# Kernel tuning notes

Hardware: AMD Instinct MI355X
Metric: run time of the kernel (lower is better)

The kernel has to match this reference:

```python
import jax, jax.numpy as jnp
import numpy as np

B, T, F = 64, 512, 512
F2, F4 = F // 2, F // 4
NUM_MOVES = 4


def setup_inputs() -> dict:
    key = jax.random.key(0)
    ks = jax.random.split(key, 12)
    s = 0.02
    return {
        "action_type_index": jax.random.randint(ks[0], (B, T), 0, 2, dtype=jnp.int32),
        "autoregressive_embedding": jax.random.normal(ks[1], (B, T, F), jnp.float32),
        "moves": jax.random.normal(ks[2], (B, T, NUM_MOVES, F2), jnp.float32),
        # guarantee each slot has at least one legal move (the torch code would NaN/error otherwise)
        "moves_mask": jax.random.bernoulli(ks[3], 0.7, (B, T, NUM_MOVES)).at[..., 0].set(True),
        "Wq1": s * jax.random.normal(ks[4], (F, F2), jnp.float32),
        "bq1": jnp.zeros((F2,), jnp.float32),
        "Wq2": s * jax.random.normal(ks[5], (F2, F4), jnp.float32),
        "bq2": jnp.zeros((F4,), jnp.float32),
        "Wk1": s * jax.random.normal(ks[6], (F2, F2), jnp.float32),
        "bk1": jnp.zeros((F2,), jnp.float32),
        "Wk2": s * jax.random.normal(ks[7], (F2, F4), jnp.float32),
        "bk2": jnp.zeros((F4,), jnp.float32),
        "Wp": s * jax.random.normal(ks[8], (F2, F), jnp.float32),
        "bp": jnp.zeros((F,), jnp.float32),
    }


def _legal_policy(logits, legal):
    # softmax over last axis that respects the legality mask, same ops as torch version
    l_min = logits.min(axis=-1, keepdims=True)
    l = jnp.where(legal, logits, l_min)
    l = l - l.max(axis=-1, keepdims=True)
    l = l * legal
    e = jnp.where(legal, jnp.exp(l), 0.0)
    return e / e.sum(axis=-1, keepdims=True)


def reference(action_type_index, autoregressive_embedding, moves, moves_mask,
              Wq1, bq1, Wq2, bq2, Wk1, bk1, Wk2, bk2, Wp, bp):
    # mask fixup: if the whole mask is empty, make everything legal (torch scalar-bool indexing)
    mask = jnp.where(moves_mask.sum() == 0, jnp.bool_(True), moves_mask)

    q = jax.nn.relu(autoregressive_embedding @ Wq1 + bq1) @ Wq2 + bq2   # [B,T,F4]
    k = jax.nn.relu(moves @ Wk1 + bk1) @ Wk2 + bk2                       # [B,T,4,F4]
    move_logits = jnp.einsum('btf,btmf->btm', q, k)                      # [B,T,4]

    move_policy = _legal_policy(move_logits, mask)                       # [B,T,4]

    # multinomial sample per (B,T) slot (deterministic key for reproducibility)
    samp_logits = jnp.where(move_policy > 0, jnp.log(move_policy), -1e30)
    idx = jax.random.categorical(jax.random.key(42), samp_logits, axis=-1)  # [B,T] int32
    move_index = idx.reshape(B, T, 1)

    # gather sampled move embedding (each slot gathers from its own 4 moves)
    move_embedding = jnp.take_along_axis(moves, idx[:, :, None, None], axis=2)[:, :, 0, :]  # [B,T,F2]
    projected_move_embedding = move_embedding @ Wp + bp                  # [B,T,F]

    valid = (action_type_index == 0)[..., None]                          # [B,T,1]
    ar_out = jnp.where(valid, autoregressive_embedding + projected_move_embedding,
                       autoregressive_embedding)
    return move_logits, move_policy, move_index, ar_out, projected_move_embedding
```

## Files before the change

kernel.cpp:

```cpp
#include <hip/hip_runtime.h>

#define B_   64
#define T_   512
#define F_   512
#define F2_  256
#define F4_  128
#define R_   32768
#define RM_  131072

typedef __attribute__((ext_vector_type(8))) short bf16x8;
typedef __attribute__((ext_vector_type(4))) float f32x4;

__device__ __forceinline__ void split_bf16(float a, unsigned short& h, unsigned short& l)
{
    unsigned x  = __float_as_uint(a);
    unsigned rh = x + 0x7FFFu + ((x >> 16) & 1u);
    unsigned short hs = (unsigned short)(rh >> 16);
    float fh = __uint_as_float((unsigned)hs << 16);
    float r  = a - fh;
    unsigned y  = __float_as_uint(r);
    unsigned rl = y + 0x7FFFu + ((y >> 16) & 1u);
    h = hs;
    l = (unsigned short)(rl >> 16);
}

template<bool TRANS>
__global__ __launch_bounds__(256)
void repack_kernel(const float* __restrict__ src, int N, int kbits,
                   unsigned short* __restrict__ hi, unsigned short* __restrict__ lo)
{
    int idx = blockIdx.x * 256 + threadIdx.x;
    int K = 1 << kbits;
    int k = idx & (K - 1);
    int n = idx >> kbits;
    float v = TRANS ? src[(size_t)k * N + n] : src[idx];
    unsigned short h, l;
    split_bf16(v, h, l);
    hi[idx] = h; lo[idx] = l;
}

#define LDSPAD 40

template<int KDIM, int NDIM, bool RELU, bool PROJ>
__global__ __launch_bounds__(256, 2)
void gemm_bf16s(const float* __restrict__ A,
                const unsigned short* __restrict__ Wh,
                const unsigned short* __restrict__ Wl,
                const float* __restrict__ bias,
                float* __restrict__ C,
                const float* __restrict__ idxf,
                const float* __restrict__ moves,
                const float* __restrict__ xres,
                const int*   __restrict__ atype,
                float* __restrict__ out_ar)
{
    __shared__ unsigned short AhS[128 * LDSPAD];
    __shared__ unsigned short AlS[128 * LDSPAD];
    __shared__ unsigned short WhS[128 * LDSPAD];
    __shared__ unsigned short WlS[128 * LDSPAD];

    const int tid  = threadIdx.x;
    const int lane = tid & 63;
    const int wid  = tid >> 6;
    const int wr   = wid >> 1;
    const int wc   = wid & 1;
    const int row0 = blockIdx.x * 128;
    const int col0 = blockIdx.y * 128;

    const int sr = tid >> 1;
    const int sc = (tid & 1) * 16;
    const float* arow;
    if constexpr (PROJ) {
        const int slot = row0 + sr;
        const int mi = (int)idxf[slot];
        arow = moves + ((size_t)slot * 4 + mi) * KDIM;
    } else {
        arow = A + (size_t)(row0 + sr) * KDIM;
    }
    const int wn = tid & 127;
    const unsigned short* wrow = ((tid >> 7) ? Wl : Wh) + (size_t)(col0 + wn) * KDIM;
    unsigned short* wdst = (tid >> 7) ? WlS : WhS;

    const int fr   = lane & 15;
    const int fkg  = (lane >> 4) * 8;
    const int aoff = (wr * 64 + fr) * LDSPAD + fkg;
    const int woff = (wc * 64 + fr) * LDSPAD + fkg;

    f32x4 acc[4][4];
#pragma unroll
    for (int i = 0; i < 4; i++)
#pragma unroll
        for (int j = 0; j < 4; j++) acc[i][j] = {0.f, 0.f, 0.f, 0.f};

    float4 pa[4];
    uint4  pw[4];
#pragma unroll
    for (int i = 0; i < 4; i++) pa[i] = *(const float4*)&arow[sc + i * 4];
#pragma unroll
    for (int i = 0; i < 4; i++) pw[i] = *(const uint4*)&wrow[i * 8];

    for (int k0 = 0; k0 < KDIM; k0 += 32) {
        {
            unsigned hw[8], lw[8];
#pragma unroll
            for (int i = 0; i < 4; i++) {
                unsigned short h0, l0, h1, l1;
                split_bf16(pa[i].x, h0, l0);
                split_bf16(pa[i].y, h1, l1);
                hw[i * 2 + 0] = (unsigned)h0 | ((unsigned)h1 << 16);
                lw[i * 2 + 0] = (unsigned)l0 | ((unsigned)l1 << 16);
                split_bf16(pa[i].z, h0, l0);
                split_bf16(pa[i].w, h1, l1);
                hw[i * 2 + 1] = (unsigned)h0 | ((unsigned)h1 << 16);
                lw[i * 2 + 1] = (unsigned)l0 | ((unsigned)l1 << 16);
            }
            *(uint4*)&AhS[sr * LDSPAD + sc]     = (uint4){hw[0], hw[1], hw[2], hw[3]};
            *(uint4*)&AhS[sr * LDSPAD + sc + 8] = (uint4){hw[4], hw[5], hw[6], hw[7]};
            *(uint4*)&AlS[sr * LDSPAD + sc]     = (uint4){lw[0], lw[1], lw[2], lw[3]};
            *(uint4*)&AlS[sr * LDSPAD + sc + 8] = (uint4){lw[4], lw[5], lw[6], lw[7]};
#pragma unroll
            for (int i = 0; i < 4; i++)
                *(uint4*)&wdst[wn * LDSPAD + i * 8] = pw[i];
        }
        __syncthreads();

        if (k0 + 32 < KDIM) {
#pragma unroll
            for (int i = 0; i < 4; i++) pa[i] = *(const float4*)&arow[k0 + 32 + sc + i * 4];
#pragma unroll
            for (int i = 0; i < 4; i++) pw[i] = *(const uint4*)&wrow[k0 + 32 + i * 8];
        }

        bf16x8 ah[4], al[4], wh[4], wl[4];
#pragma unroll
        for (int i = 0; i < 4; i++) {
            ah[i] = *(const bf16x8*)&AhS[aoff + i * 16 * LDSPAD];
            al[i] = *(const bf16x8*)&AlS[aoff + i * 16 * LDSPAD];
        }
#pragma unroll
        for (int j = 0; j < 4; j++) {
            wh[j] = *(const bf16x8*)&WhS[woff + j * 16 * LDSPAD];
            wl[j] = *(const bf16x8*)&WlS[woff + j * 16 * LDSPAD];
        }
#pragma unroll
        for (int i = 0; i < 4; i++)
#pragma unroll
            for (int j = 0; j < 4; j++) {
                acc[i][j] = __builtin_amdgcn_mfma_f32_16x16x32_bf16(ah[i], wh[j], acc[i][j], 0, 0, 0);
                acc[i][j] = __builtin_amdgcn_mfma_f32_16x16x32_bf16(ah[i], wl[j], acc[i][j], 0, 0, 0);
                acc[i][j] = __builtin_amdgcn_mfma_f32_16x16x32_bf16(al[i], wh[j], acc[i][j], 0, 0, 0);
            }
        __syncthreads();
    }

#pragma unroll
    for (int j = 0; j < 4; j++) {
        const int col = col0 + wc * 64 + j * 16 + fr;
        const float bv = bias ? bias[col] : 0.f;
#pragma unroll
        for (int i = 0; i < 4; i++) {
            const int rbase = row0 + wr * 64 + i * 16 + (lane >> 4) * 4;
#pragma unroll
            for (int r = 0; r < 4; r++) {
                float v = acc[i][j][r] + bv;
                if constexpr (RELU) v = fmaxf(v, 0.f);
                const size_t off = (size_t)(rbase + r) * NDIM + col;
                C[off] = v;
                if constexpr (PROJ) {
                    float xv = xres[off];
                    out_ar[off] = (atype[rbase + r] == 0) ? xv + v : xv;
                }
            }
        }
    }
}

__device__ __forceinline__ void threefry2x32_k42(unsigned int& x0, unsigned int& x1)
{
    const unsigned int ks0 = 0u;
    const unsigned int ks1 = 42u;
    const unsigned int ks2 = 0x1BD11BDAu ^ 42u;
    x0 += ks0; x1 += ks1;
#define TFR(r) { x0 += x1; x1 = (x1 << (r)) | (x1 >> (32 - (r))); x1 ^= x0; }
    TFR(13) TFR(15) TFR(26) TFR(6)
    x0 += ks1; x1 += ks2 + 1u;
    TFR(17) TFR(29) TFR(16) TFR(24)
    x0 += ks2; x1 += ks0 + 2u;
    TFR(13) TFR(15) TFR(26) TFR(6)
    x0 += ks0; x1 += ks1 + 3u;
    TFR(17) TFR(29) TFR(16) TFR(24)
    x0 += ks1; x1 += ks2 + 4u;
    TFR(13) TFR(15) TFR(26) TFR(6)
    x0 += ks2; x1 += ks0 + 5u;
#undef TFR
}

__global__ __launch_bounds__(256)
void logits_kernel(const float* __restrict__ u, const float* __restrict__ Hk,
                   const float* __restrict__ q, const float* __restrict__ bk2,
                   const int* __restrict__ mask,
                   float* __restrict__ out_logits, float* __restrict__ out_policy,
                   float* __restrict__ out_index, float* __restrict__ gaps,
                   int t0)
{
    const int tl   = blockIdx.x * 256 + threadIdx.x;
    const int t    = t0 + tl;
    const int slot = t >> 2;
    const int m    = t & 3;

    const float4* up = (const float4*)&u[(size_t)slot * F2_];
    const float4* hp = (const float4*)&Hk[(size_t)tl * F2_];
    double dot = 0.0;
#pragma unroll
    for (int i = 0; i < 64; i++) {
        float4 a = up[i], b = hp[i];
        dot += (double)a.x * b.x; dot += (double)a.y * b.y;
        dot += (double)a.z * b.z; dot += (double)a.w * b.w;
    }
    {
        const float4* qp = (const float4*)&q[(size_t)slot * F4_];
        const float4* bp = (const float4*)bk2;
        double qb = 0.0;
#pragma unroll
        for (int i = 0; i < 32; i++) {
            float4 a = qp[i], b = bp[i];
            qb += (double)a.x * b.x; qb += (double)a.y * b.y;
            qb += (double)a.z * b.z; qb += (double)a.w * b.w;
        }
        dot += qb;
    }

    const bool legal = (mask[t] != 0);

    double lmin = fmin(dot, __shfl_xor(dot, 1));
    lmin = fmin(lmin, __shfl_xor(lmin, 2));
    const double lm = legal ? dot : lmin;
    double lmax = fmax(lm, __shfl_xor(lm, 1));
    lmax = fmax(lmax, __shfl_xor(lmax, 2));
    const double e = legal ? exp(lm - lmax) : 0.0;
    double esum = e + __shfl_xor(e, 1);
    esum += __shfl_xor(esum, 2);
    const double policy = e / esum;

    out_logits[t] = (float)dot;
    out_policy[t] = (float)policy;

    const double sl = (policy > 0.0) ? log(policy) : -1e30;

    unsigned int x0 = 0u;
    unsigned int x1 = (unsigned int)t;
    threefry2x32_k42(x0, x1);
    const unsigned int bits = x0 ^ x1;

    const float f  = __uint_as_float(0x3f800000u | (bits >> 9)) - 1.0f;
    const float uf = fmaxf(1.17549435e-38f, f);
    const double g = -log(-log((double)uf));
    const double v = sl + g;

    int    best = m;
    double bv   = v;
    {
        double ov = __shfl_xor(bv, 1); int oi = __shfl_xor(best, 1);
        if (ov > bv || (ov == bv && oi < best)) { bv = ov; best = oi; }
        ov = __shfl_xor(bv, 2); oi = __shfl_xor(best, 2);
        if (ov > bv || (ov == bv && oi < best)) { bv = ov; best = oi; }
    }

    double a1 = fmax(v, __shfl_xor(v, 1));
    double b1 = fmin(v, __shfl_xor(v, 1));
    double a2 = __shfl_xor(a1, 2);
    double b2 = __shfl_xor(b1, 2);
    double top2 = (a1 >= a2) ? fmax(a2, b1) : fmax(a1, b2);
    double top1 = fmax(a1, a2);

    if (m == 0) {
        out_index[slot] = (float)best;
        gaps[slot] = (float)(top1 - top2);
    }
}

#define TAU_ 3e-3f

__global__ __launch_bounds__(1024)
void compact_kernel(const float* __restrict__ gaps,
                    int* __restrict__ cnt, int* __restrict__ list)
{
    __shared__ int c;
    if (threadIdx.x == 0) c = 0;
    __syncthreads();
    for (int s = threadIdx.x; s < R_; s += 1024) {
        if (gaps[s] < TAU_) list[atomicAdd(&c, 1)] = s;
    }
    __syncthreads();
    if (threadIdx.x == 0) *cnt = c;
}

__global__ __launch_bounds__(256)
void cleanup2_kernel(const float* __restrict__ x, const float* __restrict__ moves,
                     const int* __restrict__ mask,
                     const float* __restrict__ Wq1, const float* __restrict__ bq1,
                     const float* __restrict__ Wq2, const float* __restrict__ bq2,
                     const float* __restrict__ Wk1, const float* __restrict__ bk1,
                     const float* __restrict__ Wk2, const float* __restrict__ bk2,
                     const int* __restrict__ cnt, const int* __restrict__ list,
                     float* __restrict__ out_index)
{
    __shared__ float  xs[512];
    __shared__ float  mvs[1024];
    __shared__ float  ws[16 * 256];
    __shared__ double h1q[256];
    __shared__ double h1k[4][256];
    __shared__ double qv[128];
    __shared__ double kv[4][128];
    __shared__ double wred[8];

    const int j = threadIdx.x;
    const int n = *cnt;

    for (int ii = blockIdx.x; ii < n; ii += gridDim.x) {
        const int s = list[ii];
        __syncthreads();

        *(float2*)&xs[j * 2] = *(const float2*)&x[(size_t)s * F_ + j * 2];
        ((float4*)mvs)[j] = ((const float4*)&moves[(size_t)s * 4 * F2_])[j];

        double a0 = 0.0, a1 = 0.0;
        for (int c0 = 0; c0 < 512; c0 += 16) {
            __syncthreads();
#pragma unroll
            for (int u = 0; u < 4; u++) {
                int idx = u * 256 + j;
                int r = idx >> 6, c4 = (idx & 63) * 4;
                *(float4*)&ws[r * 256 + c4] = *(const float4*)&Wq1[(size_t)(c0 + r) * F2_ + c4];
            }
            __syncthreads();
#pragma unroll
            for (int c = 0; c < 16; c += 2) {
                a0 += (double)xs[c0 + c]     * (double)ws[c * 256 + j];
                a1 += (double)xs[c0 + c + 1] * (double)ws[(c + 1) * 256 + j];
            }
        }
        h1q[j] = fmax(a0 + a1 + (double)bq1[j], 0.0);

        double q0 = 0.0, q1 = 0.0;
        for (int c0 = 0; c0 < 256; c0 += 32) {
            __syncthreads();
#pragma unroll
            for (int u = 0; u < 4; u++) {
                int idx = u * 256 + j;
                int r = idx >> 5, c4 = (idx & 31) * 4;
                *(float4*)&ws[r * 128 + c4] = *(const float4*)&Wq2[(size_t)(c0 + r) * F4_ + c4];
            }
            __syncthreads();
            if (j < 128) {
#pragma unroll
                for (int c = 0; c < 32; c += 2) {
                    q0 += h1q[c0 + c]     * (double)ws[c * 128 + j];
                    q1 += h1q[c0 + c + 1] * (double)ws[(c + 1) * 128 + j];
                }
            }
        }
        if (j < 128) qv[j] = q0 + q1 + (double)bq2[j];

        double k0 = 0.0, k1 = 0.0, k2 = 0.0, k3 = 0.0;
        for (int c0 = 0; c0 < 256; c0 += 16) {
            __syncthreads();
#pragma unroll
            for (int u = 0; u < 4; u++) {
                int idx = u * 256 + j;
                int r = idx >> 6, c4 = (idx & 63) * 4;
                *(float4*)&ws[r * 256 + c4] = *(const float4*)&Wk1[(size_t)(c0 + r) * F2_ + c4];
            }
            __syncthreads();
#pragma unroll
            for (int c = 0; c < 16; c++) {
                double w = (double)ws[c * 256 + j];
                k0 += (double)mvs[0 * 256 + c0 + c] * w;
                k1 += (double)mvs[1 * 256 + c0 + c] * w;
                k2 += (double)mvs[2 * 256 + c0 + c] * w;
                k3 += (double)mvs[3 * 256 + c0 + c] * w;
            }
        }
        h1k[0][j] = fmax(k0 + (double)bk1[j], 0.0);
        h1k[1][j] = fmax(k1 + (double)bk1[j], 0.0);
        h1k[2][j] = fmax(k2 + (double)bk1[j], 0.0);
        h1k[3][j] = fmax(k3 + (double)bk1[j], 0.0);

        const int jj = j & 127, mh = j >> 7;
        double v0 = 0.0, v1 = 0.0;
        for (int c0 = 0; c0 < 256; c0 += 32) {
            __syncthreads();
#pragma unroll
            for (int u = 0; u < 4; u++) {
                int idx = u * 256 + j;
                int r = idx >> 5, c4 = (idx & 31) * 4;
                *(float4*)&ws[r * 128 + c4] = *(const float4*)&Wk2[(size_t)(c0 + r) * F4_ + c4];
            }
            __syncthreads();
#pragma unroll
            for (int c = 0; c < 32; c++) {
                double w = (double)ws[c * 128 + jj];
                v0 += h1k[mh][c0 + c]     * w;
                v1 += h1k[mh + 2][c0 + c] * w;
            }
        }
        kv[mh][jj]     = v0 + (double)bk2[jj];
        kv[mh + 2][jj] = v1 + (double)bk2[jj];
        __syncthreads();

        {
            const int w = j >> 6, l = j & 63;
            double d = qv[l] * kv[w][l] + qv[l + 64] * kv[w][l + 64];
#pragma unroll
            for (int o = 32; o; o >>= 1) d += __shfl_xor(d, o);
            if (l == 0) wred[w] = d;
        }
        __syncthreads();

        if (j == 0) {
            double dotS[4];
#pragma unroll
            for (int mv = 0; mv < 4; mv++) dotS[mv] = wred[mv];
            double lmin = dotS[0];
#pragma unroll
            for (int mv = 1; mv < 4; mv++) lmin = fmin(lmin, dotS[mv]);
            double lm[4]; bool lg[4];
            double lmax = -1e300;
#pragma unroll
            for (int mv = 0; mv < 4; mv++) {
                lg[mv] = (mask[(size_t)s * 4 + mv] != 0);
                lm[mv] = lg[mv] ? dotS[mv] : lmin;
                lmax = fmax(lmax, lm[mv]);
            }
            double e[4]; double esum = 0.0;
#pragma unroll
            for (int mv = 0; mv < 4; mv++) {
                e[mv] = lg[mv] ? exp(lm[mv] - lmax) : 0.0;
                esum += e[mv];
            }
            int best = -1; double bv = -1e308;
#pragma unroll
            for (int mv = 0; mv < 4; mv++) {
                double pol = e[mv] / esum;
                double sl = (pol > 0.0) ? log(pol) : -1e30;
                unsigned xx0 = 0u, xx1 = (unsigned)(s * 4 + mv);
                threefry2x32_k42(xx0, xx1);
                unsigned bits = xx0 ^ xx1;
                float fu = __uint_as_float(0x3f800000u | (bits >> 9)) - 1.0f;
                float uf = fmaxf(1.17549435e-38f, fu);
                double g = -log(-log((double)uf));
                double v = sl + g;
                if (v > bv) { bv = v; best = mv; }
            }
            out_index[s] = (float)best;
        }
    }
}

template<int KDIM>
__global__ __launch_bounds__(256, 3)
void mlp2_kernel(const float* __restrict__ A,
                 const float* __restrict__ W1, const float* __restrict__ b1,
                 const float* __restrict__ W2, const float* __restrict__ b2,
                 float* __restrict__ out)
{
    __shared__ float H[32][260];
    __shared__ float As[32][20];
    __shared__ float Bs[4096];

    const int tid  = threadIdx.x;
    const int row0 = blockIdx.x * 32;
    const int tx   = tid & 31;
    const int ty   = tid >> 5;

    float acc[4][8];
#pragma unroll
    for (int i = 0; i < 4; i++)
#pragma unroll
        for (int j = 0; j < 8; j++) acc[i][j] = 0.f;

    for (int k0 = 0; k0 < KDIM; k0 += 16) {
        {
            int r = tid >> 3;
            int c = (tid & 7) * 2;
            float2 v = *(const float2*)&A[(size_t)(row0 + r) * KDIM + k0 + c];
            *(float2*)&As[r][c] = v;
        }
        {
            int kk = tid >> 4;
            int c0 = (tid & 15) * 16;
            const float* src = &W1[(size_t)(k0 + kk) * F2_ + c0];
            float* dst = &Bs[kk * F2_ + c0];
#pragma unroll
            for (int j = 0; j < 4; j++) ((float4*)dst)[j] = ((const float4*)src)[j];
        }
        __syncthreads();
#pragma unroll
        for (int kk = 0; kk < 16; kk += 4) {
            float4 a[4];
#pragma unroll
            for (int i = 0; i < 4; i++) a[i] = *(const float4*)&As[ty * 4 + i][kk];
#pragma unroll
            for (int u = 0; u < 4; u++) {
                float4 w0 = *(const float4*)&Bs[(kk + u) * F2_ + tx * 8];
                float4 w1 = *(const float4*)&Bs[(kk + u) * F2_ + tx * 8 + 4];
#pragma unroll
                for (int i = 0; i < 4; i++) {
                    float av = ((const float*)&a[i])[u];
                    acc[i][0] += av * w0.x; acc[i][1] += av * w0.y;
                    acc[i][2] += av * w0.z; acc[i][3] += av * w0.w;
                    acc[i][4] += av * w1.x; acc[i][5] += av * w1.y;
                    acc[i][6] += av * w1.z; acc[i][7] += av * w1.w;
                }
            }
        }
        __syncthreads();
    }
    {
        float4 b1a = *(const float4*)&b1[tx * 8];
        float4 b1b = *(const float4*)&b1[tx * 8 + 4];
        const float bv[8] = {b1a.x, b1a.y, b1a.z, b1a.w, b1b.x, b1b.y, b1b.z, b1b.w};
#pragma unroll
        for (int i = 0; i < 4; i++) {
            float4 h0, h1;
            h0.x = fmaxf(acc[i][0] + bv[0], 0.f);
            h0.y = fmaxf(acc[i][1] + bv[1], 0.f);
            h0.z = fmaxf(acc[i][2] + bv[2], 0.f);
            h0.w = fmaxf(acc[i][3] + bv[3], 0.f);
            h1.x = fmaxf(acc[i][4] + bv[4], 0.f);
            h1.y = fmaxf(acc[i][5] + bv[5], 0.f);
            h1.z = fmaxf(acc[i][6] + bv[6], 0.f);
            h1.w = fmaxf(acc[i][7] + bv[7], 0.f);
            *(float4*)&H[ty * 4 + i][tx * 8]     = h0;
            *(float4*)&H[ty * 4 + i][tx * 8 + 4] = h1;
        }
    }
    __syncthreads();

    float acc2[4][4];
#pragma unroll
    for (int i = 0; i < 4; i++)
#pragma unroll
        for (int j = 0; j < 4; j++) acc2[i][j] = 0.f;

    for (int k0 = 0; k0 < F2_; k0 += 32) {
        {
            int kk = tid >> 3;
            int c0 = (tid & 7) * 16;
            const float* src = &W2[(size_t)(k0 + kk) * F4_ + c0];
            float* dst = &Bs[kk * F4_ + c0];
#pragma unroll
            for (int j = 0; j < 4; j++) ((float4*)dst)[j] = ((const float4*)src)[j];
        }
        __syncthreads();
#pragma unroll
        for (int kk = 0; kk < 32; kk += 4) {
            float4 h[4];
#pragma unroll
            for (int i = 0; i < 4; i++) h[i] = *(const float4*)&H[ty * 4 + i][k0 + kk];
#pragma unroll
            for (int u = 0; u < 4; u++) {
                float4 w = *(const float4*)&Bs[(kk + u) * F4_ + tx * 4];
#pragma unroll
                for (int i = 0; i < 4; i++) {
                    float hv = ((const float*)&h[i])[u];
                    acc2[i][0] += hv * w.x; acc2[i][1] += hv * w.y;
                    acc2[i][2] += hv * w.z; acc2[i][3] += hv * w.w;
                }
            }
        }
        __syncthreads();
    }
    {
        float4 bb = *(const float4*)&b2[tx * 4];
#pragma unroll
        for (int i = 0; i < 4; i++) {
            float4 o;
            o.x = acc2[i][0] + bb.x;
            o.y = acc2[i][1] + bb.y;
            o.z = acc2[i][2] + bb.z;
            o.w = acc2[i][3] + bb.w;
            *(float4*)&out[(size_t)(row0 + ty * 4 + i) * F4_ + tx * 4] = o;
        }
    }
}

__global__ __launch_bounds__(256)
void logits_sample_kernel(const float* __restrict__ Q, const float* __restrict__ Kv,
                          const int* __restrict__ mask,
                          float* __restrict__ out_logits, float* __restrict__ out_policy,
                          float* __restrict__ out_index)
{
    const int t    = blockIdx.x * 256 + threadIdx.x;
    const int slot = t >> 2;
    const int m    = t & 3;

    const float4* qp = (const float4*)&Q[(size_t)slot * F4_];
    const float4* kp = (const float4*)&Kv[(size_t)t * F4_];
    double dot = 0.0;
#pragma unroll
    for (int i = 0; i < 32; i++) {
        float4 a = qp[i], b = kp[i];
        dot += (double)a.x * b.x; dot += (double)a.y * b.y;
        dot += (double)a.z * b.z; dot += (double)a.w * b.w;
    }

    const bool legal = (mask[t] != 0);

    double lmin = fmin(dot, __shfl_xor(dot, 1));
    lmin = fmin(lmin, __shfl_xor(lmin, 2));
    const double lm = legal ? dot : lmin;
    double lmax = fmax(lm, __shfl_xor(lm, 1));
    lmax = fmax(lmax, __shfl_xor(lmax, 2));
    const double e = legal ? exp(lm - lmax) : 0.0;
    double esum = e + __shfl_xor(e, 1);
    esum += __shfl_xor(esum, 2);
    const double policy = e / esum;

    out_logits[t] = (float)dot;
    out_policy[t] = (float)policy;

    const double sl = (policy > 0.0) ? log(policy) : -1e30;

    unsigned int x0 = 0u;
    unsigned int x1 = (unsigned int)t;
    threefry2x32_k42(x0, x1);
    const unsigned int bits = x0 ^ x1;

    const float f  = __uint_as_float(0x3f800000u | (bits >> 9)) - 1.0f;
    const float uf = fmaxf(1.17549435e-38f, f);
    const double g = -log(-log((double)uf));
    const double v = sl + g;

    int    best = m;
    double bv   = v;
    {
        double ov = __shfl_xor(bv, 1); int oi = __shfl_xor(best, 1);
        if (ov > bv || (ov == bv && oi < best)) { bv = ov; best = oi; }
        ov = __shfl_xor(bv, 2); oi = __shfl_xor(best, 2);
        if (ov > bv || (ov == bv && oi < best)) { bv = ov; best = oi; }
    }
    if (m == 0) out_index[slot] = (float)best;
}

__global__ __launch_bounds__(256, 3)
void proj_kernel(const float* __restrict__ moves, const float* __restrict__ idxf,
                 const float* __restrict__ Wp, const float* __restrict__ bp,
                 const float* __restrict__ x, const int* __restrict__ atype,
                 float* __restrict__ out_ar, float* __restrict__ out_proj)
{
    __shared__ float As[32][260];
    __shared__ float Bs[32 * 128];

    const int tid  = threadIdx.x;
    const int row0 = blockIdx.x * 32;
    const int col0 = blockIdx.y * 128;
    const int tx   = tid & 31;
    const int ty   = tid >> 5;

#pragma unroll
    for (int it = 0; it < 8; it++) {
        int r = (tid >> 6) + it * 4;
        int c = (tid & 63) * 4;
        int slot = row0 + r;
        int mi = (int)idxf[slot];
        float4 v = *(const float4*)&moves[((size_t)slot * 4 + mi) * F2_ + c];
        *(float4*)&As[r][c] = v;
    }
    __syncthreads();

    float acc[4][4];
#pragma unroll
    for (int i = 0; i < 4; i++)
#pragma unroll
        for (int j = 0; j < 4; j++) acc[i][j] = 0.f;

    for (int k0 = 0; k0 < F2_; k0 += 32) {
        {
            int kk = tid >> 3;
            int c0 = (tid & 7) * 16;
            const float* src = &Wp[(size_t)(k0 + kk) * F_ + col0 + c0];
            float* dst = &Bs[kk * 128 + c0];
#pragma unroll
            for (int j = 0; j < 4; j++) ((float4*)dst)[j] = ((const float4*)src)[j];
        }
        __syncthreads();
#pragma unroll
        for (int kk = 0; kk < 32; kk += 4) {
            float4 h[4];
#pragma unroll
            for (int i = 0; i < 4; i++) h[i] = *(const float4*)&As[ty * 4 + i][k0 + kk];
#pragma unroll
            for (int u = 0; u < 4; u++) {
                float4 w = *(const float4*)&Bs[(kk + u) * 128 + tx * 4];
#pragma unroll
                for (int i = 0; i < 4; i++) {
                    float hv = ((const float*)&h[i])[u];
                    acc[i][0] += hv * w.x; acc[i][1] += hv * w.y;
                    acc[i][2] += hv * w.z; acc[i][3] += hv * w.w;
                }
            }
        }
        __syncthreads();
    }

    float4 bb = *(const float4*)&bp[col0 + tx * 4];
#pragma unroll
    for (int i = 0; i < 4; i++) {
        int row = row0 + ty * 4 + i;
        float4 p;
        p.x = acc[i][0] + bb.x;
        p.y = acc[i][1] + bb.y;
        p.z = acc[i][2] + bb.z;
        p.w = acc[i][3] + bb.w;
        size_t off = (size_t)row * F_ + col0 + tx * 4;
        *(float4*)&out_proj[off] = p;
        float4 a = *(const float4*)&x[off];
        bool valid = (atype[row] == 0);
        float4 r4;
        r4.x = valid ? a.x + p.x : a.x;
        r4.y = valid ? a.y + p.y : a.y;
        r4.z = valid ? a.z + p.z : a.z;
        r4.w = valid ? a.w + p.w : a.w;
        *(float4*)&out_ar[off] = r4;
    }
}

extern "C" void kernel_launch(void* const* d_in, const int* in_sizes, int n_in,
                              void* d_out, int out_size, void* d_ws, size_t ws_size,
                              hipStream_t stream)
{
    (void)in_sizes; (void)n_in; (void)out_size;

    const int*   atype = (const int*)d_in[0];
    const float* x     = (const float*)d_in[1];
    const float* moves = (const float*)d_in[2];
    const int*   mask  = (const int*)d_in[3];
    const float* Wq1   = (const float*)d_in[4];
    const float* bq1   = (const float*)d_in[5];
    const float* Wq2   = (const float*)d_in[6];
    const float* bq2   = (const float*)d_in[7];
    const float* Wk1   = (const float*)d_in[8];
    const float* bk1   = (const float*)d_in[9];
    const float* Wk2   = (const float*)d_in[10];
    const float* bk2   = (const float*)d_in[11];
    const float* Wp    = (const float*)d_in[12];
    const float* bp    = (const float*)d_in[13];

    float* out_logits = (float*)d_out;
    float* out_policy = out_logits + RM_;
    float* out_index  = out_policy + RM_;
    float* out_ar     = out_index + R_;
    float* out_proj   = out_ar + (size_t)R_ * F_;

    const size_t WS_NEED = (size_t)786432 * 2 + (size_t)R_ * 4;

    if (d_ws != nullptr && ws_size >= WS_NEED) {
        unsigned short* wq1h = (unsigned short*)d_ws;
        unsigned short* wq1l = wq1h + 131072;
        unsigned short* wq2h = wq1l + 131072;
        unsigned short* wq2l = wq2h + 32768;
        unsigned short* wk1h = wq2l + 32768;
        unsigned short* wk1l = wk1h + 65536;
        unsigned short* wk2h = wk1l + 65536;
        unsigned short* wk2l = wk2h + 32768;
        unsigned short* wph  = wk2l + 32768;
        unsigned short* wpl  = wph + 131072;
        float* gaps = (float*)(wpl + 131072);

        float* Hq = out_ar;
        float* qv = out_ar + 8388608;
        float* uv = out_proj;
        float* Hk = out_ar;
        int* cl_cnt  = (int*)(out_ar + 12582912);
        int* cl_list = cl_cnt + 16;

        repack_kernel<true ><<<512, 256, 0, stream>>>(Wq1, F2_, 9, wq1h, wq1l);
        repack_kernel<true ><<<128, 256, 0, stream>>>(Wq2, F4_, 8, wq2h, wq2l);
        repack_kernel<true ><<<256, 256, 0, stream>>>(Wk1, F2_, 8, wk1h, wk1l);
        repack_kernel<false><<<128, 256, 0, stream>>>(Wk2, F4_, 7, wk2h, wk2l);
        repack_kernel<true ><<<512, 256, 0, stream>>>(Wp,  F_,  8, wph,  wpl);

        dim3 g1(R_ / 128, 2);
        gemm_bf16s<512, 256, true,  false><<<g1, 256, 0, stream>>>(
            x, wq1h, wq1l, bq1, Hq, nullptr, nullptr, nullptr, nullptr, nullptr);
        dim3 g2(R_ / 128, 1);
        gemm_bf16s<256, 128, false, false><<<g2, 256, 0, stream>>>(
            Hq, wq2h, wq2l, bq2, qv, nullptr, nullptr, nullptr, nullptr, nullptr);
        dim3 g3(R_ / 128, 2);
        gemm_bf16s<128, 256, false, false><<<g3, 256, 0, stream>>>(
            qv, wk2h, wk2l, nullptr, uv, nullptr, nullptr, nullptr, nullptr, nullptr);

        for (int qi = 0; qi < 4; qi++) {
            const float* mseg = moves + (size_t)qi * 32768 * F2_;
            gemm_bf16s<256, 256, true, false><<<g3, 256, 0, stream>>>(
                mseg, wk1h, wk1l, bk1, Hk, nullptr, nullptr, nullptr, nullptr, nullptr);
            logits_kernel<<<128, 256, 0, stream>>>(
                uv, Hk, qv, bk2, mask, out_logits, out_policy, out_index, gaps, qi * 32768);
        }

        compact_kernel<<<1, 1024, 0, stream>>>(gaps, cl_cnt, cl_list);
        cleanup2_kernel<<<128, 256, 0, stream>>>(
            x, moves, mask, Wq1, bq1, Wq2, bq2, Wk1, bk1, Wk2, bk2,
            cl_cnt, cl_list, out_index);

        dim3 gp(R_ / 128, 4);
        gemm_bf16s<256, 512, false, true><<<gp, 256, 0, stream>>>(
            nullptr, wph, wpl, bp, out_proj, out_index, moves, x, atype, out_ar);
    } else {
        float* Q  = out_proj;
        float* Kv = out_ar;

        mlp2_kernel<F_><<<R_ / 32, 256, 0, stream>>>(x, Wq1, bq1, Wq2, bq2, Q);
        mlp2_kernel<F2_><<<RM_ / 32, 256, 0, stream>>>(moves, Wk1, bk1, Wk2, bk2, Kv);
        logits_sample_kernel<<<RM_ / 256, 256, 0, stream>>>(Q, Kv, mask,
                                                            out_logits, out_policy, out_index);
        dim3 pgrid(R_ / 32, 4);
        proj_kernel<<<pgrid, 256, 0, stream>>>(moves, out_index, Wp, bp, x, atype,
                                               out_ar, out_proj);
    }
}
```

Baseline: 822.4 us.

## Double-buffer GEMM LDS tiles and fuse key-hidden dot into moves GEMM epilogue

The bf16-split GEMM now double-buffers its LDS tiles with a single barrier per K-step, so global loads and conversion for the next tile overlap the MFMAs on the current one. The moves GEMM gets a DOT epilogue that applies ReLU and bias and dots each row with the precomputed u vector in double precision. It writes per-column-block partial sums instead of materialising the hidden activations. This removes the four-chunk loop of GEMM plus logits kernels and the round trip of the 128K×256 hidden tensor through memory, replacing them with one GEMM and a light finalize kernel. Doubling LDS raises shared-memory use per block, which may limit occupancy.

```diff
diff --git a/kernel.cpp b/kernel.cpp
--- a/kernel.cpp
+++ b/kernel.cpp
@@ -41,7 +41,7 @@
 
 #define LDSPAD 40
 
-template<int KDIM, int NDIM, bool RELU, bool PROJ>
+template<int KDIM, int NDIM, bool RELU, bool PROJ, bool DOT>
 __global__ __launch_bounds__(256, 2)
 void gemm_bf16s(const float* __restrict__ A,
                 const unsigned short* __restrict__ Wh,
@@ -52,12 +52,15 @@
                 const float* __restrict__ moves,
                 const float* __restrict__ xres,
                 const int*   __restrict__ atype,
-                float* __restrict__ out_ar)
-{
-    __shared__ unsigned short AhS[128 * LDSPAD];
-    __shared__ unsigned short AlS[128 * LDSPAD];
-    __shared__ unsigned short WhS[128 * LDSPAD];
-    __shared__ unsigned short WlS[128 * LDSPAD];
+                float* __restrict__ out_ar,
+                const float* __restrict__ udot,
+                double* __restrict__ part)
+{
+    constexpr int BUFE = 128 * LDSPAD;
+    __shared__ __align__(16) unsigned short AhS[2 * BUFE];
+    __shared__ __align__(16) unsigned short AlS[2 * BUFE];
+    __shared__ __align__(16) unsigned short WhS[2 * BUFE];
+    __shared__ __align__(16) unsigned short WlS[2 * BUFE];
 
     const int tid  = threadIdx.x;
     const int lane = tid & 63;
@@ -79,78 +82,144 @@
     }
     const int wn = tid & 127;
     const unsigned short* wrow = ((tid >> 7) ? Wl : Wh) + (size_t)(col0 + wn) * KDIM;
-    unsigned short* wdst = (tid >> 7) ? WlS : WhS;
 
     const int fr   = lane & 15;
     const int fkg  = (lane >> 4) * 8;
     const int aoff = (wr * 64 + fr) * LDSPAD + fkg;
     const int woff = (wc * 64 + fr) * LDSPAD + fkg;
 
-    f32x4 acc[4][4];
-#pragma unroll
-    for (int i = 0; i < 4; i++)
-#pragma unroll
-        for (int j = 0; j < 4; j++) acc[i][j] = {0.f, 0.f, 0.f, 0.f};
-
     float4 pa[4];
     uint4  pw[4];
-#pragma unroll
-    for (int i = 0; i < 4; i++) pa[i] = *(const float4*)&arow[sc + i * 4];
-#pragma unroll
-    for (int i = 0; i < 4; i++) pw[i] = *(const uint4*)&wrow[i * 8];
-
-    for (int k0 = 0; k0 < KDIM; k0 += 32) {
-        {
-            unsigned hw[8], lw[8];
-#pragma unroll
-            for (int i = 0; i < 4; i++) {
-                unsigned short h0, l0, h1, l1;
-                split_bf16(pa[i].x, h0, l0);
-                split_bf16(pa[i].y, h1, l1);
-                hw[i * 2 + 0] = (unsigned)h0 | ((unsigned)h1 << 16);
-                lw[i * 2 + 0] = (unsigned)l0 | ((unsigned)l1 << 16);
-                split_bf16(pa[i].z, h0, l0);
-                split_bf16(pa[i].w, h1, l1);
-                hw[i * 2 + 1] = (unsigned)h0 | ((unsigned)h1 << 16);
-                lw[i * 2 + 1] = (unsigned)l0 | ((unsigned)l1 << 16);
-            }
-            *(uint4*)&AhS[sr * LDSPAD + sc]     = (uint4){hw[0], hw[1], hw[2], hw[3]};
-            *(uint4*)&AhS[sr * LDSPAD + sc + 8] = (uint4){hw[4], hw[5], hw[6], hw[7]};
-            *(uint4*)&AlS[sr * LDSPAD + sc]     = (uint4){lw[0], lw[1], lw[2], lw[3]};
-            *(uint4*)&AlS[sr * LDSPAD + sc + 8] = (uint4){lw[4], lw[5], lw[6], lw[7]};
+
+    auto issue_loads = [&](int k0) {
+#pragma unroll
+        for (int i = 0; i < 4; i++) pa[i] = *(const float4*)&arow[k0 + sc + i * 4];
+#pragma unroll
+        for (int i = 0; i < 4; i++) pw[i] = *(const uint4*)&wrow[k0 + i * 8];
+    };
+
+    auto convert_write = [&](int b) {
+        unsigned hw[8], lw[8];
+#pragma unroll
+        for (int i = 0; i < 4; i++) {
+            unsigned short h0, l0, h1, l1;
+            split_bf16(pa[i].x, h0, l0);
+            split_bf16(pa[i].y, h1, l1);
+            hw[i * 2 + 0] = (unsigned)h0 | ((unsigned)h1 << 16);
+            lw[i * 2 + 0] = (unsigned)l0 | ((unsigned)l1 << 16);
+            split_bf16(pa[i].z, h0, l0);
+            split_bf16(pa[i].w, h1, l1);
+            hw[i * 2 + 1] = (unsigned)h0 | ((unsigned)h1 << 16);
+            lw[i * 2 + 1] = (unsigned)l0 | ((unsigned)l1 << 16);
+        }
+        unsigned short* ahp = AhS + b * BUFE;
+        unsigned short* alp = AlS + b * BUFE;
+        *(uint4*)&ahp[sr * LDSPAD + sc]     = (uint4){hw[0], hw[1], hw[2], hw[3]};
+        *(uint4*)&ahp[sr * LDSPAD + sc + 8] = (uint4){hw[4], hw[5], hw[6], hw[7]};
+        *(uint4*)&alp[sr * LDSPAD + sc]     = (uint4){lw[0], lw[1], lw[2], lw[3]};
+        *(uint4*)&alp[sr * LDSPAD + sc + 8] = (uint4){lw[4], lw[5], lw[6], lw[7]};
+        unsigned short* wp = ((tid >> 7) ? WlS : WhS) + b * BUFE;
+#pragma unroll
+        for (int i = 0; i < 4; i++)
+            *(uint4*)&wp[wn * LDSPAD + i * 8] = pw[i];
+    };
+
+    f32x4 acc[4][4];
+#pragma unroll
+    for (int i = 0; i < 4; i++)
+#pragma unroll
+        for (int j = 0; j < 4; j++) acc[i][j] = {0.f, 0.f, 0.f, 0.f};
+
+    issue_loads(0);
+    convert_write(0);
+    issue_loads(32);
+    asm volatile("s_waitcnt lgkmcnt(0)" ::: "memory");
+    __builtin_amdgcn_s_barrier();
+    __builtin_amdgcn_sched_barrier(0);
+
+    constexpr int NT = KDIM / 32;
+    for (int t = 0; t < NT; ++t) {
+        const int cur = t & 1;
+        const unsigned short* ab  = AhS + cur * BUFE;
+        const unsigned short* lb  = AlS + cur * BUFE;
+        const unsigned short* whb = WhS + cur * BUFE;
+        const unsigned short* wlb = WlS + cur * BUFE;
+
+        bf16x8 fah[4], fal[4], fwh[4], fwl[4];
+#pragma unroll
+        for (int i = 0; i < 4; i++) {
+            fah[i] = *(const bf16x8*)&ab[aoff + i * 16 * LDSPAD];
+            fal[i] = *(const bf16x8*)&lb[aoff + i * 16 * LDSPAD];
+        }
+#pragma unroll
+        for (int j = 0; j < 4; j++) {
+            fwh[j] = *(const bf16x8*)&whb[woff + j * 16 * LDSPAD];
+            fwl[j] = *(const bf16x8*)&wlb[woff + j * 16 * LDSPAD];
+        }
+#pragma unroll
+        for (int i = 0; i < 4; i++)
+#pragma unroll
+            for (int j = 0; j < 4; j++) {
+                acc[i][j] = __builtin_amdgcn_mfma_f32_16x16x32_bf16(fah[i], fwh[j], acc[i][j], 0, 0, 0);
+                acc[i][j] = __builtin_amdgcn_mfma_f32_16x16x32_bf16(fah[i], fwl[j], acc[i][j], 0, 0, 0);
+                acc[i][j] = __builtin_amdgcn_mfma_f32_16x16x32_bf16(fal[i], fwh[j], acc[i][j], 0, 0, 0);
+            }
+        __builtin_amdgcn_sched_barrier(0);
+
+        if (t + 1 < NT) convert_write((t + 1) & 1);
+        if (t + 2 < NT) issue_loads((t + 2) * 32);
+
+        asm volatile("s_waitcnt lgkmcnt(0)" ::: "memory");
+        __builtin_amdgcn_s_barrier();
+        __builtin_amdgcn_sched_barrier(0);
+    }
+
+    if constexpr (DOT) {
+        double pv[4][4];
+#pragma unroll
+        for (int i = 0; i < 4; i++) {
+            const int lrow = wr * 64 + i * 16 + ((lane >> 4) << 2);
+            const int slot = (row0 + lrow) >> 2;
+            double pr0 = 0.0, pr1 = 0.0, pr2 = 0.0, pr3 = 0.0;
+#pragma unroll
+            for (int j = 0; j < 4; j++) {
+                const int col = col0 + wc * 64 + j * 16 + fr;
+                const double u = (double)udot[(size_t)slot * F2_ + col];
+                const float bv = bias[col];
+                pr0 += (double)fmaxf(acc[i][j][0] + bv, 0.f) * u;
+                pr1 += (double)fmaxf(acc[i][j][1] + bv, 0.f) * u;
+                pr2 += (double)fmaxf(acc[i][j][2] + bv, 0.f) * u;
+                pr3 += (double)fmaxf(acc[i][j][3] + bv, 0.f) * u;
+            }
+            pv[i][0] = pr0; pv[i][1] = pr1; pv[i][2] = pr2; pv[i][3] = pr3;
+        }
+#pragma unroll
+        for (int o = 1; o <= 8; o <<= 1)
 #pragma unroll
             for (int i = 0; i < 4; i++)
-                *(uint4*)&wdst[wn * LDSPAD + i * 8] = pw[i];
-        }
-        __syncthreads();
-
-        if (k0 + 32 < KDIM) {
-#pragma unroll
-            for (int i = 0; i < 4; i++) pa[i] = *(const float4*)&arow[k0 + 32 + sc + i * 4];
-#pragma unroll
-            for (int i = 0; i < 4; i++) pw[i] = *(const uint4*)&wrow[k0 + 32 + i * 8];
-        }
-
-        bf16x8 ah[4], al[4], wh[4], wl[4];
-#pragma unroll
-        for (int i = 0; i < 4; i++) {
-            ah[i] = *(const bf16x8*)&AhS[aoff + i * 16 * LDSPAD];
-            al[i] = *(const bf16x8*)&AlS[aoff + i * 16 * LDSPAD];
-        }
-#pragma unroll
-        for (int j = 0; j < 4; j++) {
-            wh[j] = *(const bf16x8*)&WhS[woff + j * 16 * LDSPAD];
-            wl[j] = *(const bf16x8*)&WlS[woff + j * 16 * LDSPAD];
-        }
-#pragma unroll
-        for (int i = 0; i < 4; i++)
-#pragma unroll
-            for (int j = 0; j < 4; j++) {
-                acc[i][j] = __builtin_amdgcn_mfma_f32_16x16x32_bf16(ah[i], wh[j], acc[i][j], 0, 0, 0);
-                acc[i][j] = __builtin_amdgcn_mfma_f32_16x16x32_bf16(ah[i], wl[j], acc[i][j], 0, 0, 0);
-                acc[i][j] = __builtin_amdgcn_mfma_f32_16x16x32_bf16(al[i], wh[j], acc[i][j], 0, 0, 0);
-            }
-        __syncthreads();
+#pragma unroll
+                for (int r = 0; r < 4; r++)
+                    pv[i][r] += __shfl_xor(pv[i][r], o);
+
+        double* red = (double*)AhS;
+        if (wc == 0 && fr == 0) {
+#pragma unroll
+            for (int i = 0; i < 4; i++)
+#pragma unroll
+                for (int r = 0; r < 4; r++)
+                    red[wr * 64 + i * 16 + ((lane >> 4) << 2) + r] = pv[i][r];
+        }
+        __syncthreads();
+        if (wc == 1 && fr == 0) {
+#pragma unroll
+            for (int i = 0; i < 4; i++)
+#pragma unroll
+                for (int r = 0; r < 4; r++)
+                    red[wr * 64 + i * 16 + ((lane >> 4) << 2) + r] += pv[i][r];
+        }
+        __syncthreads();
+        if (tid < 128) part[(size_t)blockIdx.y * RM_ + row0 + tid] = red[tid];
+        return;
     }
 
 #pragma unroll
@@ -196,27 +265,17 @@
 }
 
 __global__ __launch_bounds__(256)
-void logits_kernel(const float* __restrict__ u, const float* __restrict__ Hk,
-                   const float* __restrict__ q, const float* __restrict__ bk2,
-                   const int* __restrict__ mask,
-                   float* __restrict__ out_logits, float* __restrict__ out_policy,
-                   float* __restrict__ out_index, float* __restrict__ gaps,
-                   int t0)
-{
-    const int tl   = blockIdx.x * 256 + threadIdx.x;
-    const int t    = t0 + tl;
+void logits_finalize(const double* __restrict__ part,
+                     const float* __restrict__ q, const float* __restrict__ bk2,
+                     const int* __restrict__ mask,
+                     float* __restrict__ out_logits, float* __restrict__ out_policy,
+                     float* __restrict__ out_index, float* __restrict__ gaps)
+{
+    const int t    = blockIdx.x * 256 + threadIdx.x;
     const int slot = t >> 2;
     const int m    = t & 3;
 
-    const float4* up = (const float4*)&u[(size_t)slot * F2_];
-    const float4* hp = (const float4*)&Hk[(size_t)tl * F2_];
-    double dot = 0.0;
-#pragma unroll
-    for (int i = 0; i < 64; i++) {
-        float4 a = up[i], b = hp[i];
-        dot += (double)a.x * b.x; dot += (double)a.y * b.y;
-        dot += (double)a.z * b.z; dot += (double)a.w * b.w;
-    }
+    double dot = part[t] + part[RM_ + t];
     {
         const float4* qp = (const float4*)&q[(size_t)slot * F4_];
         const float4* bp = (const float4*)bk2;
@@ -768,11 +827,11 @@
         unsigned short* wpl  = wph + 131072;
         float* gaps = (float*)(wpl + 131072);
 
-        float* Hq = out_ar;
-        float* qv = out_ar + 8388608;
-        float* uv = out_proj;
-        float* Hk = out_ar;
-        int* cl_cnt  = (int*)(out_ar + 12582912);
+        float*  Hq   = out_ar;
+        float*  qv   = out_ar + 8388608;
+        float*  uv   = out_proj;
+        double* part = (double*)(out_ar + 12582912);
+        int* cl_cnt  = (int*)(out_ar + 13631488);
         int* cl_list = cl_cnt + 16;
 
         repack_kernel<true ><<<512, 256, 0, stream>>>(Wq1, F2_, 9, wq1h, wq1l);
@@ -782,22 +841,21 @@
         repack_kernel<true ><<<512, 256, 0, stream>>>(Wp,  F_,  8, wph,  wpl);
 
         dim3 g1(R_ / 128, 2);
-        gemm_bf16s<512, 256, true,  false><<<g1, 256, 0, stream>>>(
-            x, wq1h, wq1l, bq1, Hq, nullptr, nullptr, nullptr, nullptr, nullptr);
+        gemm_bf16s<512, 256, true,  false, false><<<g1, 256, 0, stream>>>(
+            x, wq1h, wq1l, bq1, Hq, nullptr, nullptr, nullptr, nullptr, nullptr, nullptr, nullptr);
         dim3 g2(R_ / 128, 1);
-        gemm_bf16s<256, 128, false, false><<<g2, 256, 0, stream>>>(
-            Hq, wq2h, wq2l, bq2, qv, nullptr, nullptr, nullptr, nullptr, nullptr);
+        gemm_bf16s<256, 128, false, false, false><<<g2, 256, 0, stream>>>(
+            Hq, wq2h, wq2l, bq2, qv, nullptr, nullptr, nullptr, nullptr, nullptr, nullptr, nullptr);
         dim3 g3(R_ / 128, 2);
-        gemm_bf16s<128, 256, false, false><<<g3, 256, 0, stream>>>(
-            qv, wk2h, wk2l, nullptr, uv, nullptr, nullptr, nullptr, nullptr, nullptr);
-
-        for (int qi = 0; qi < 4; qi++) {
-            const float* mseg = moves + (size_t)qi * 32768 * F2_;
-            gemm_bf16s<256, 256, true, false><<<g3, 256, 0, stream>>>(
-                mseg, wk1h, wk1l, bk1, Hk, nullptr, nullptr, nullptr, nullptr, nullptr);
-            logits_kernel<<<128, 256, 0, stream>>>(
-                uv, Hk, qv, bk2, mask, out_logits, out_policy, out_index, gaps, qi * 32768);
-        }
+        gemm_bf16s<128, 256, false, false, false><<<g3, 256, 0, stream>>>(
+            qv, wk2h, wk2l, nullptr, uv, nullptr, nullptr, nullptr, nullptr, nullptr, nullptr, nullptr);
+
+        dim3 gk(RM_ / 128, 2);
+        gemm_bf16s<256, 256, true, false, true><<<gk, 256, 0, stream>>>(
+            moves, wk1h, wk1l, bk1, nullptr, nullptr, nullptr, nullptr, nullptr, nullptr, uv, part);
+
+        logits_finalize<<<RM_ / 256, 256, 0, stream>>>(
+            part, qv, bk2, mask, out_logits, out_policy, out_index, gaps);
 
         compact_kernel<<<1, 1024, 0, stream>>>(gaps, cl_cnt, cl_list);
         cleanup2_kernel<<<128, 256, 0, stream>>>(
@@ -805,8 +863,8 @@
             cl_cnt, cl_list, out_index);
 
         dim3 gp(R_ / 128, 4);
-        gemm_bf16s<256, 512, false, true><<<gp, 256, 0, stream>>>(
-            nullptr, wph, wpl, bp, out_proj, out_index, moves, x, atype, out_ar);
+        gemm_bf16s<256, 512, false, true, false><<<gp, 256, 0, stream>>>(
+            nullptr, wph, wpl, bp, out_proj, out_index, moves, x, atype, out_ar, nullptr, nullptr);
     } else {
         float* Q  = out_proj;
         float* Kv = out_ar;
```

After: 731.9 us. 1.12x faster.
